# Kernel optimization log

Measured on AMD Instinct MI355X. Metric: run time of the kernel, lower is better.

## Reference

```python
import jax, jax.numpy as jnp
from jax import lax
import numpy as np

BOHR = 0.52917721067  # Angstrom per Bohr (au.BOHR)
DAMP_MUTUAL = 0.39
DAMP_FIELD = 0.7
N_ITER = 7  # fixed-point iterations for induced dipoles


def setup_inputs() -> dict:
    key = jax.random.key(0)
    N = 100000
    deg = 32
    E = N * deg
    k1, k2, k3, k4, k5, k6, k7 = jax.random.split(key, 7)
    edge_src = jax.random.randint(k1, (E,), 0, N)
    edge_dst = jax.random.randint(k2, (E,), 0, N)
    # realistic interatomic distances in [1, 6] Angstrom (avoid r ~ 0)
    distances = 1.0 + 5.0 * jax.random.uniform(k3, (E,), dtype=jnp.float32)
    u = jax.random.normal(k4, (E, 3), dtype=jnp.float32)
    u = u / jnp.linalg.norm(u, axis=-1, keepdims=True)
    vec = u * distances[:, None]  # consistent |vec| == distances
    polarisability = 0.5 + 1.5 * jax.random.uniform(k5, (N,), dtype=jnp.float32)
    charges = 0.3 * jax.random.normal(k6, (N,), dtype=jnp.float32)
    species = jax.random.randint(k7, (N,), 1, 10)
    return {
        "species": species,
        "edge_src": edge_src,
        "edge_dst": edge_dst,
        "distances": distances,
        "vec": vec,
        "polarisability": polarisability,
        "charges": charges,
    }


def reference(species, edge_src, edge_dst, distances, vec, polarisability, charges):
    N = polarisability.shape[0]
    # convert to atomic units
    rij = distances / BOHR                      # [E]
    vec_ij = vec / BOHR                         # [E,3]
    pol = polarisability.reshape(-1) / BOHR**3  # [N]

    # Thole damping: u_ij^3 = r^3 / sqrt(alpha_i * alpha_j)
    alpha_ij = pol[edge_src] * pol[edge_dst]
    uij3 = rij**3 / jnp.sqrt(alpha_ij)
    exp_m = jnp.exp(-DAMP_MUTUAL * uij3)
    l3_m = 1.0 - exp_m
    l5_m = 1.0 - (1.0 + DAMP_MUTUAL * uij3) * exp_m
    l3_f = 1.0 - jnp.exp(-DAMP_FIELD * uij3)

    inv_r3 = 1.0 / rij**3
    inv_r5 = inv_r3 / rij**2

    # permanent (charge) electric field at src atoms, Thole-damped
    e_edges = (l3_f * charges[edge_dst] * inv_r3)[:, None] * vec_ij  # [E,3]
    E0 = jax.ops.segment_sum(e_edges, edge_src, num_segments=N)      # [N,3]

    alpha = pol[:, None]  # isotropic polarisability [N,1]

    def matvec(mu):
        # Thole-damped dipole-dipole interaction tensor applied to mu: (T mu)_i
        mu_d = mu[edge_dst]                                   # [E,3]
        dot = jnp.sum(vec_ij * mu_d, axis=-1)                 # [E]
        t = (l3_m * inv_r3)[:, None] * mu_d \
            - (3.0 * l5_m * inv_r5 * dot)[:, None] * vec_ij   # [E,3]
        return jax.ops.segment_sum(t, edge_src, num_segments=N)

    # iterative induced dipoles: mu = alpha * (E0 - T mu)
    mu0 = alpha * E0

    def step(mu, _):
        return alpha * (E0 - matvec(mu)), None

    mu, _ = lax.scan(step, mu0, None, length=N_ITER)

    # per-atom polarisation energy: -1/2 mu . E0
    energy = -0.5 * jnp.sum(mu * E0, axis=-1)  # [N]
    return energy
```

## Files before the change

kernel.cpp:

```cpp
#include <hip/hip_runtime.h>
#include <hip/hip_fp16.h>


static constexpr float INV_B  = 1.0f / 0.52917721067f;
static constexpr float INV_B3 = INV_B * INV_B * INV_B;
static constexpr float DM = 0.39f;
static constexpr float DF = 0.7f;
static constexpr int   NITER = 7;
#define STAGE 4096
#define BUILD_T 512
#define CHUNK 8192
#define MAXBUCK 512

__device__ inline unsigned packh2(float a, float b) {
    return (unsigned)__half_as_ushort(__float2half_rn(a)) |
           ((unsigned)__half_as_ushort(__float2half_rn(b)) << 16);
}
__device__ inline float unph_lo(unsigned u) {
    return __half2float(__ushort_as_half((unsigned short)(u & 0xFFFFu)));
}
__device__ inline float unph_hi(unsigned u) {
    return __half2float(__ushort_as_half((unsigned short)(u >> 16)));
}


__global__ void bhist_kernel(const int* __restrict__ esrc, int* __restrict__ btot,
                             int E, int nbuck, int chunk)
{
    __shared__ int cnt[MAXBUCK];
    int tid = threadIdx.x, blk = blockIdx.x;
    for (int b = tid; b < nbuck; b += blockDim.x) cnt[b] = 0;
    __syncthreads();
    int lo = blk * chunk, hi = min(E, lo + chunk);
    for (int i = lo + tid; i < hi; i += blockDim.x)
        atomicAdd(&cnt[esrc[i] >> 8], 1);
    __syncthreads();
    for (int b = tid; b < nbuck; b += blockDim.x)
        if (cnt[b]) atomicAdd(&btot[b], cnt[b]);
}


__global__ void bktptr_kernel(const int* __restrict__ btot,
                              int* __restrict__ bktptr, int* __restrict__ gcur,
                              int* __restrict__ rowptr,
                              int nbuck, int N, int E)
{
    __shared__ int wsum[8];
    int tid = threadIdx.x;
    int lane = tid & 63, wav = tid >> 6;
    int v = (tid < nbuck) ? btot[tid] : 0;
    int x = v;
    #pragma unroll
    for (int off = 1; off < 64; off <<= 1) {
        int t = __shfl_up(x, off);
        if (lane >= off) x += t;
    }
    if (lane == 63) wsum[wav] = x;
    __syncthreads();
    if (tid < 8) {
        int w = wsum[tid];
        #pragma unroll
        for (int off = 1; off < 8; off <<= 1) {
            int t = __shfl_up(w, off, 8);
            if (tid >= off) w += t;
        }
        wsum[tid] = w;
    }
    __syncthreads();
    int base = (wav > 0) ? wsum[wav - 1] : 0;
    if (tid < nbuck) {
        int beg = x + base - v;
        bktptr[tid] = beg;
        gcur[tid]   = beg;
    }
    if (tid == 0) {
        bktptr[nbuck] = E;
        rowptr[N] = E;
    }
}


__global__ __launch_bounds__(BUILD_T)
void build_kernel(const int* __restrict__ esrc, const int* __restrict__ edst,
                  const float* __restrict__ dist, const float* __restrict__ vec,
                  const float* __restrict__ pol, const float* __restrict__ chg,
                  int* __restrict__ gcur,
                  uint4* __restrict__ recs, int E, int nbuck, int chunk)
{
    __shared__ uint4 stg[STAGE];
    __shared__ unsigned short sbuck[STAGE];
    __shared__ int wbase[MAXBUCK];
    __shared__ int shist[MAXBUCK];
    __shared__ int sbase[MAXBUCK];
    __shared__ int scur[MAXBUCK];
    __shared__ int wsum[8];
    int tid = threadIdx.x, blk = blockIdx.x;
    int lane = tid & 63, wav = tid >> 6;
    int lo = blk * chunk, hi = min(E, lo + chunk), cnt = hi - lo;

    int nsb = (cnt + STAGE - 1) / STAGE;
    for (int sb = 0; sb < nsb; ++sb) {
        int s0 = sb * STAGE, s1 = min(cnt, s0 + STAGE), scnt = s1 - s0;
        if (tid < nbuck) shist[tid] = 0;
        __syncthreads();
        for (int i = s0 + tid; i < s1; i += BUILD_T)
            atomicAdd(&shist[esrc[lo + i] >> 8], 1);
        __syncthreads();
        int v = (tid < nbuck) ? shist[tid] : 0;
        int x = v;
        #pragma unroll
        for (int off = 1; off < 64; off <<= 1) {
            int t = __shfl_up(x, off);
            if (lane >= off) x += t;
        }
        if (lane == 63) wsum[wav] = x;
        __syncthreads();
        if (tid < 8) {
            int w = wsum[tid];
            #pragma unroll
            for (int off = 1; off < 8; off <<= 1) {
                int t = __shfl_up(w, off, 8);
                if (tid >= off) w += t;
            }
            wsum[tid] = w;
        }
        __syncthreads();
        int base = (wav > 0) ? wsum[wav - 1] : 0;
        if (tid < nbuck) {
            int ex = x + base - v;
            sbase[tid] = ex;
            scur[tid]  = ex;
            wbase[tid] = v ? atomicAdd(&gcur[tid], v) : 0;
        }
        __syncthreads();
        for (int i = s0 + tid; i < s1; i += BUILD_T) {
            int gi = lo + i;
            int s = esrc[gi], d = edst[gi];
            int b = s >> 8;
            float r  = dist[gi] * INV_B;
            float vx = vec[3*gi+0] * INV_B;
            float vy = vec[3*gi+1] * INV_B;
            float vz = vec[3*gi+2] * INV_B;
            float ps = pol[s] * INV_B3;
            float pd = pol[d] * INV_B3;
            float r2 = r * r;
            float r3 = r2 * r;
            float u  = r3 * rsqrtf(ps * pd);
            float em = __expf(-DM * u);
            float l3m = 1.0f - em;
            float l5m = 1.0f - (1.0f + DM * u) * em;
            float inv_r3 = 1.0f / r3;
            float inv_r5 = inv_r3 / r2;
            float c1 = l3m * inv_r3;
            float sw = sqrtf(3.0f * l5m * inv_r5);
            float ec = (1.0f - __expf(-DF * u)) * chg[d] * inv_r3;
            float g  = ec / sw;
            uint4 rc;
            rc.x = (unsigned)(d | ((s & 255) << 20));
            rc.y = __float_as_uint(c1);
            rc.z = packh2(sw * vx, sw * vy);
            rc.w = packh2(sw * vz, g);
            int sl = atomicAdd(&scur[b], 1);
            stg[sl]   = rc;
            sbuck[sl] = (unsigned short)b;
        }
        __syncthreads();
        for (int k = tid; k < scnt; k += BUILD_T) {
            int b = sbuck[k];
            recs[wbase[b] + (k - sbase[b])] = stg[k];
        }
        __syncthreads();
    }
}


__global__ void sort_kernel(const int* __restrict__ bktptr,
                            const uint4* __restrict__ recs_raw,
                            unsigned* __restrict__ srt,
                            int* __restrict__ rowptr, const float* __restrict__ pol,
                            float4* __restrict__ E0, float4* __restrict__ mu, int N)
{
    __shared__ int hist[256];
    __shared__ int cur[256];
    __shared__ float acc[256 * 3];
    __shared__ int wsum4[4];
    int tid = threadIdx.x, b = blockIdx.x;
    int lane = tid & 63, wav = tid >> 6;
    int j0 = bktptr[b], j1 = bktptr[b + 1];
    if (tid < 256) hist[tid] = 0;
    for (int k = tid; k < 768; k += blockDim.x) acc[k] = 0.f;
    __syncthreads();
    for (int j = j0 + tid; j < j1; j += blockDim.x)
        atomicAdd(&hist[recs_raw[j].x >> 20], 1);
    __syncthreads();
    int v = (tid < 256) ? hist[tid] : 0;
    int x = v;
    #pragma unroll
    for (int off = 1; off < 64; off <<= 1) {
        int t = __shfl_up(x, off);
        if (lane >= off) x += t;
    }
    if (lane == 63 && wav < 4) wsum4[wav] = x;
    __syncthreads();
    if (tid < 4) {
        int w = wsum4[tid];
        #pragma unroll
        for (int off = 1; off < 4; off <<= 1) {
            int t = __shfl_up(w, off, 4);
            if (tid >= off) w += t;
        }
        wsum4[tid] = w;
    }
    __syncthreads();
    if (tid < 256) {
        int base = (wav > 0) ? wsum4[wav - 1] : 0;
        int beg = j0 + x + base - v;
        cur[tid] = beg;
        int row = b * 256 + tid;
        if (row < N) rowptr[row] = beg;
    }
    __syncthreads();
    for (int j = j0 + tid; j < j1; j += blockDim.x) {
        uint4 rc = recs_raw[j];
        int lr = (int)(rc.x >> 20);
        int slot = atomicAdd(&cur[lr], 1);
        float c1 = __uint_as_float(rc.y);
        float wx = unph_lo(rc.z), wy = unph_hi(rc.z);
        float wz = unph_lo(rc.w), g  = unph_hi(rc.w);
        srt[3*slot+0] = rc.x;
        srt[3*slot+1] = packh2(c1, wx);
        srt[3*slot+2] = packh2(wy, wz);
        atomicAdd(&acc[lr*3+0], g * wx);
        atomicAdd(&acc[lr*3+1], g * wy);
        atomicAdd(&acc[lr*3+2], g * wz);
    }
    __syncthreads();
    if (tid < 256) {
        int row = b * 256 + tid;
        if (row < N) {
            float ax = acc[tid*3], ay = acc[tid*3+1], az = acc[tid*3+2];
            E0[row] = make_float4(ax, ay, az, 0.f);
            float a = pol[row] * INV_B3;
            mu[row] = make_float4(a * ax, a * ay, a * az, 0.f);
        }
    }
}


__global__ void mvg_kernel(const int* __restrict__ rowptr,
                           const unsigned* __restrict__ srt, const float4* __restrict__ E0,
                           const float* __restrict__ pol,
                           const float4* __restrict__ mu_in, float4* __restrict__ mu_out,
                           float* __restrict__ energy, int N, int final_iter)
{
    int tid  = threadIdx.x;
    int lane = tid & 15;
    int row  = (blockIdx.x * blockDim.x + tid) >> 4;
    if (row >= N) return;
    int r0 = rowptr[row], r1 = rowptr[row + 1];
    float ax = 0.f, ay = 0.f, az = 0.f;
    for (int j = r0 + lane; j < r1; j += 16) {
        unsigned pk = srt[3*j+0];
        unsigned w0 = srt[3*j+1];
        unsigned w1 = srt[3*j+2];
        float4 m = mu_in[pk & 0xFFFFF];
        float c1 = unph_lo(w0);
        float wx = unph_hi(w0), wy = unph_lo(w1), wz = unph_hi(w1);
        float dot = wx * m.x + wy * m.y + wz * m.z;
        ax += c1 * m.x - dot * wx;
        ay += c1 * m.y - dot * wy;
        az += c1 * m.z - dot * wz;
    }
    for (int msk = 8; msk >= 1; msk >>= 1) {
        ax += __shfl_xor(ax, msk);
        ay += __shfl_xor(ay, msk);
        az += __shfl_xor(az, msk);
    }
    if (lane == 0) {
        float4 e0 = E0[row];
        float a = pol[row] * INV_B3;
        float mx = a * (e0.x - ax);
        float my = a * (e0.y - ay);
        float mz = a * (e0.z - az);
        mu_out[row] = make_float4(mx, my, mz, 0.f);
        if (final_iter)
            energy[row] = -0.5f * (mx * e0.x + my * e0.y + mz * e0.z);
    }
}


__global__ void fb_e0_kernel(const int* esrc, const int* edst, const float* dist,
                             const float* vec, const float* pol, const float* chg,
                             float4* E0, int E)
{
    int e = blockIdx.x * blockDim.x + threadIdx.x;
    if (e >= E) return;
    int s = esrc[e], d = edst[e];
    float r  = dist[e] * INV_B;
    float vx = vec[3*e+0]*INV_B, vy = vec[3*e+1]*INV_B, vz = vec[3*e+2]*INV_B;
    float r3 = r*r*r;
    float u  = r3 * rsqrtf(pol[s]*INV_B3 * pol[d]*INV_B3);
    float ec = (1.0f - __expf(-DF*u)) * chg[d] / r3;
    atomicAdd(&E0[s].x, ec*vx); atomicAdd(&E0[s].y, ec*vy); atomicAdd(&E0[s].z, ec*vz);
}

__global__ void fb_init_kernel(const float* pol, const float4* E0, float4* mu, float4* acc, int N)
{
    int i = blockIdx.x * blockDim.x + threadIdx.x;
    if (i >= N) return;
    float a = pol[i]*INV_B3; float4 e0 = E0[i];
    mu[i]  = make_float4(a*e0.x, a*e0.y, a*e0.z, 0.f);
    acc[i] = make_float4(0.f,0.f,0.f,0.f);
}

__global__ void fb_matvec_kernel(const int* esrc, const int* edst, const float* dist,
                                 const float* vec, const float* pol,
                                 const float4* mu, float4* acc, int E)
{
    int e = blockIdx.x * blockDim.x + threadIdx.x;
    if (e >= E) return;
    int s = esrc[e], d = edst[e];
    float r  = dist[e]*INV_B;
    float vx = vec[3*e+0]*INV_B, vy = vec[3*e+1]*INV_B, vz = vec[3*e+2]*INV_B;
    float r2 = r*r, r3 = r2*r;
    float u  = r3 * rsqrtf(pol[s]*INV_B3 * pol[d]*INV_B3);
    float em = __expf(-DM*u);
    float c1 = (1.0f - em) / r3;
    float c2 = 3.0f * (1.0f - (1.0f + DM*u)*em) / (r3*r2);
    float4 m = mu[d];
    float k = c2 * (vx*m.x + vy*m.y + vz*m.z);
    atomicAdd(&acc[s].x, c1*m.x - k*vx);
    atomicAdd(&acc[s].y, c1*m.y - k*vy);
    atomicAdd(&acc[s].z, c1*m.z - k*vz);
}

__global__ void fb_update_kernel(const float* pol, const float4* E0, float4* acc,
                                 float4* mu, float* energy, int N, int final_iter)
{
    int i = blockIdx.x * blockDim.x + threadIdx.x;
    if (i >= N) return;
    float a = pol[i]*INV_B3; float4 e0 = E0[i]; float4 ac = acc[i];
    float mx = a*(e0.x-ac.x), my = a*(e0.y-ac.y), mz = a*(e0.z-ac.z);
    mu[i]  = make_float4(mx,my,mz,0.f);
    acc[i] = make_float4(0.f,0.f,0.f,0.f);
    if (final_iter) energy[i] = -0.5f*(mx*e0.x + my*e0.y + mz*e0.z);
}


static inline size_t align_up(size_t x, size_t a) { return (x + a - 1) & ~(a - 1); }

extern "C" void kernel_launch(void* const* d_in, const int* in_sizes, int n_in,
                              void* d_out, int out_size, void* d_ws, size_t ws_size,
                              hipStream_t stream)
{
    const int*   esrc = (const int*)  d_in[1];
    const int*   edst = (const int*)  d_in[2];
    const float* dist = (const float*)d_in[3];
    const float* vec  = (const float*)d_in[4];
    const float* pol  = (const float*)d_in[5];
    const float* chg  = (const float*)d_in[6];
    const int E = in_sizes[1];
    const int N = in_sizes[5];
    float* out = (float*)d_out;

    const int nbuck = (N + 255) >> 8;
    const int nblk  = (E + CHUNK - 1) / CHUNK;

    char* ws = (char*)d_ws;
    size_t off = 0;
    auto carve = [&](size_t bytes) { size_t o = off; off = align_up(off + bytes, 256); return o; };
    size_t o_bkt    = carve((size_t)(nbuck + 1) * 4);
    size_t o_btot   = carve((size_t)nbuck * 4);
    size_t o_gcur   = carve((size_t)nbuck * 4);
    size_t o_E0     = carve((size_t)N * 16);
    size_t o_mua    = carve((size_t)N * 16);
    size_t o_mub    = carve((size_t)N * 16);
    size_t o_rowptr = carve((size_t)(N + 1) * 4);
    size_t o_recs   = carve((size_t)E * 16);
    size_t o_srt    = carve((size_t)E * 12);
    size_t need = off;

    bool ok = (ws_size >= need) && (nbuck <= MAXBUCK) && (nbuck >= 1) && (N < (1 << 20));

    if (ok) {
        int*      bktptr = (int*)     (ws + o_bkt);
        int*      btot   = (int*)     (ws + o_btot);
        int*      gcur   = (int*)     (ws + o_gcur);
        float4*   E0     = (float4*)  (ws + o_E0);
        float4*   mu_a   = (float4*)  (ws + o_mua);
        float4*   mu_b   = (float4*)  (ws + o_mub);
        int*      rowptr = (int*)     (ws + o_rowptr);
        uint4*    recs   = (uint4*)   (ws + o_recs);
        unsigned* srt    = (unsigned*)(ws + o_srt);

        hipMemsetAsync(btot, 0, (size_t)nbuck * 4, stream);
        bhist_kernel<<<nblk, BUILD_T, 0, stream>>>(esrc, btot, E, nbuck, CHUNK);
        bktptr_kernel<<<1, 512, 0, stream>>>(btot, bktptr, gcur, rowptr, nbuck, N, E);
        build_kernel<<<nblk, BUILD_T, 0, stream>>>(esrc, edst, dist, vec, pol, chg,
                                                   gcur, recs, E, nbuck, CHUNK);
        sort_kernel<<<nbuck, 512, 0, stream>>>(bktptr, recs, srt, rowptr,
                                               pol, E0, mu_a, N);

        const int NG16 = (N + 15) / 16;
        float4* min_ = mu_a; float4* mout_ = mu_b;
        for (int it = 0; it < NITER; ++it) {
            mvg_kernel<<<NG16, 256, 0, stream>>>(rowptr, srt, E0, pol,
                                                 min_, mout_, out, N, it == NITER - 1);
            float4* t = min_; min_ = mout_; mout_ = t;
        }
    } else {
        float4* E0  = (float4*)(ws);
        float4* mu  = (float4*)(ws + (size_t)N * 16);
        float4* acc = (float4*)(ws + (size_t)N * 32);
        const int EB = 256, NB = 256;
        const int EG = (E + EB - 1) / EB;
        const int NG = (N + NB - 1) / NB;
        hipMemsetAsync(E0, 0, (size_t)N * 16, stream);
        fb_e0_kernel<<<EG, EB, 0, stream>>>(esrc, edst, dist, vec, pol, chg, E0, E);
        fb_init_kernel<<<NG, NB, 0, stream>>>(pol, E0, mu, acc, N);
        for (int it = 0; it < NITER; ++it) {
            fb_matvec_kernel<<<EG, EB, 0, stream>>>(esrc, edst, dist, vec, pol, mu, acc, E);
            fb_update_kernel<<<NG, NB, 0, stream>>>(pol, E0, acc, mu, out, N, it == NITER - 1);
        }
    }
}
```

Baseline: 334.9 us.

## Store sorted edge records as 16-byte uint4 and simplify build scatter

```diff
diff --git a/kernel.cpp b/kernel.cpp
--- a/kernel.cpp
+++ b/kernel.cpp
@@ -9,7 +9,7 @@
 static constexpr int   NITER = 7;
 #define STAGE 4096
 #define BUILD_T 512
-#define CHUNK 8192
+#define CHUNK 4096
 #define MAXBUCK 512
 
 __device__ inline unsigned packh2(float a, float b) {
@@ -88,10 +88,9 @@
                   uint4* __restrict__ recs, int E, int nbuck, int chunk)
 {
     __shared__ uint4 stg[STAGE];
-    __shared__ unsigned short sbuck[STAGE];
     __shared__ int wbase[MAXBUCK];
     __shared__ int shist[MAXBUCK];
-    __shared__ int sbase[MAXBUCK];
+    __shared__ int sbase[MAXBUCK + 1];
     __shared__ int scur[MAXBUCK];
     __shared__ int wsum[8];
     int tid = threadIdx.x, blk = blockIdx.x;
@@ -132,6 +131,7 @@
             scur[tid]  = ex;
             wbase[tid] = v ? atomicAdd(&gcur[tid], v) : 0;
         }
+        if (tid == 0) sbase[nbuck] = scnt;
         __syncthreads();
         for (int i = s0 + tid; i < s1; i += BUILD_T) {
             int gi = lo + i;
@@ -161,13 +161,17 @@
             rc.z = packh2(sw * vx, sw * vy);
             rc.w = packh2(sw * vz, g);
             int sl = atomicAdd(&scur[b], 1);
-            stg[sl]   = rc;
-            sbuck[sl] = (unsigned short)b;
+            stg[sl] = rc;
         }
         __syncthreads();
         for (int k = tid; k < scnt; k += BUILD_T) {
-            int b = sbuck[k];
-            recs[wbase[b] + (k - sbase[b])] = stg[k];
+            uint4 rc = stg[k];
+            int loB = 0, hiB = nbuck;
+            while (hiB - loB > 1) {
+                int mid = (loB + hiB) >> 1;
+                if (sbase[mid] <= k) loB = mid; else hiB = mid;
+            }
+            recs[wbase[loB] + (k - sbase[loB])] = rc;
         }
         __syncthreads();
     }
@@ -176,7 +180,7 @@
 
 __global__ void sort_kernel(const int* __restrict__ bktptr,
                             const uint4* __restrict__ recs_raw,
-                            unsigned* __restrict__ srt,
+                            uint4* __restrict__ srt,
                             int* __restrict__ rowptr, const float* __restrict__ pol,
                             float4* __restrict__ E0, float4* __restrict__ mu, int N)
 {
@@ -190,8 +194,9 @@
     if (tid < 256) hist[tid] = 0;
     for (int k = tid; k < 768; k += blockDim.x) acc[k] = 0.f;
     __syncthreads();
+    const unsigned* recx = (const unsigned*)recs_raw;
     for (int j = j0 + tid; j < j1; j += blockDim.x)
-        atomicAdd(&hist[recs_raw[j].x >> 20], 1);
+        atomicAdd(&hist[recx[4 * (size_t)j] >> 20], 1);
     __syncthreads();
     int v = (tid < 256) ? hist[tid] : 0;
     int x = v;
@@ -224,12 +229,9 @@
         uint4 rc = recs_raw[j];
         int lr = (int)(rc.x >> 20);
         int slot = atomicAdd(&cur[lr], 1);
-        float c1 = __uint_as_float(rc.y);
+        srt[slot] = rc;
         float wx = unph_lo(rc.z), wy = unph_hi(rc.z);
         float wz = unph_lo(rc.w), g  = unph_hi(rc.w);
-        srt[3*slot+0] = rc.x;
-        srt[3*slot+1] = packh2(c1, wx);
-        srt[3*slot+2] = packh2(wy, wz);
         atomicAdd(&acc[lr*3+0], g * wx);
         atomicAdd(&acc[lr*3+1], g * wy);
         atomicAdd(&acc[lr*3+2], g * wz);
@@ -248,7 +250,7 @@
 
 
 __global__ void mvg_kernel(const int* __restrict__ rowptr,
-                           const unsigned* __restrict__ srt, const float4* __restrict__ E0,
+                           const uint4* __restrict__ srt, const float4* __restrict__ E0,
                            const float* __restrict__ pol,
                            const float4* __restrict__ mu_in, float4* __restrict__ mu_out,
                            float* __restrict__ energy, int N, int final_iter)
@@ -260,12 +262,10 @@
     int r0 = rowptr[row], r1 = rowptr[row + 1];
     float ax = 0.f, ay = 0.f, az = 0.f;
     for (int j = r0 + lane; j < r1; j += 16) {
-        unsigned pk = srt[3*j+0];
-        unsigned w0 = srt[3*j+1];
-        unsigned w1 = srt[3*j+2];
-        float4 m = mu_in[pk & 0xFFFFF];
-        float c1 = unph_lo(w0);
-        float wx = unph_hi(w0), wy = unph_lo(w1), wz = unph_hi(w1);
+        uint4 rc = srt[j];
+        float4 m = mu_in[rc.x & 0xFFFFF];
+        float c1 = __uint_as_float(rc.y);
+        float wx = unph_lo(rc.z), wy = unph_hi(rc.z), wz = unph_lo(rc.w);
         float dot = wx * m.x + wy * m.y + wz * m.z;
         ax += c1 * m.x - dot * wx;
         ay += c1 * m.y - dot * wy;
@@ -377,21 +377,21 @@
     size_t o_mub    = carve((size_t)N * 16);
     size_t o_rowptr = carve((size_t)(N + 1) * 4);
     size_t o_recs   = carve((size_t)E * 16);
-    size_t o_srt    = carve((size_t)E * 12);
+    size_t o_srt    = carve((size_t)E * 16);
     size_t need = off;
 
     bool ok = (ws_size >= need) && (nbuck <= MAXBUCK) && (nbuck >= 1) && (N < (1 << 20));
 
     if (ok) {
-        int*      bktptr = (int*)     (ws + o_bkt);
-        int*      btot   = (int*)     (ws + o_btot);
-        int*      gcur   = (int*)     (ws + o_gcur);
-        float4*   E0     = (float4*)  (ws + o_E0);
-        float4*   mu_a   = (float4*)  (ws + o_mua);
-        float4*   mu_b   = (float4*)  (ws + o_mub);
-        int*      rowptr = (int*)     (ws + o_rowptr);
-        uint4*    recs   = (uint4*)   (ws + o_recs);
-        unsigned* srt    = (unsigned*)(ws + o_srt);
+        int*    bktptr = (int*)   (ws + o_bkt);
+        int*    btot   = (int*)   (ws + o_btot);
+        int*    gcur   = (int*)   (ws + o_gcur);
+        float4* E0     = (float4*)(ws + o_E0);
+        float4* mu_a   = (float4*)(ws + o_mua);
+        float4* mu_b   = (float4*)(ws + o_mub);
+        int*    rowptr = (int*)   (ws + o_rowptr);
+        uint4*  recs   = (uint4*) (ws + o_recs);
+        uint4*  srt    = (uint4*) (ws + o_srt);
 
         hipMemsetAsync(btot, 0, (size_t)nbuck * 4, stream);
         bhist_kernel<<<nblk, BUILD_T, 0, stream>>>(esrc, btot, E, nbuck, CHUNK);
```

Result: slower. 350.8 us (+4.7%).
